# Performance work log

Hardware: AMD Instinct MI355X
Metric: run time of the kernel (lower is better)

The kernel has to match this reference:

```python
import jax, jax.numpy as jnp
import numpy as np
from jax import lax

SCALES = (1, 4, 16, 64)
EPS = 1e-5
B, S, D, H, R, FF = 4, 1024, 512, 8, 4, 2048
C = D // len(SCALES)  # channels per temporal scale


def _ln(x, g, b):
    mu = jnp.mean(x, -1, keepdims=True)
    var = jnp.mean(jnp.square(x - mu), -1, keepdims=True)
    return (x - mu) * lax.rsqrt(var + EPS) * g + b


def _interp_linear(y, L_out):
    # y: [B, C, L_in]; torch F.interpolate(mode='linear', align_corners=False)
    L_in = y.shape[-1]
    if L_in == L_out:
        return y
    pos = (jnp.arange(L_out, dtype=jnp.float32) + 0.5) * (L_in / L_out) - 0.5
    pos = jnp.clip(pos, 0.0, L_in - 1)
    lo = jnp.floor(pos).astype(jnp.int32)
    hi = jnp.minimum(lo + 1, L_in - 1)
    w = (pos - lo.astype(jnp.float32))
    return y[..., lo] * (1.0 - w) + y[..., hi] * w


def _conv1d(x, w, b, stride):
    # x: [B, Cin, L], w: [Cout, Cin, K]
    y = lax.conv_general_dilated(x, w, window_strides=(stride,), padding='VALID',
                                 dimension_numbers=('NCH', 'OIH', 'NCH'))
    return y + b[None, :, None]


def setup_inputs() -> dict:
    key = jax.random.key(0)
    ks = jax.random.split(key, 40)
    n = lambda k, shp, s=0.02: jax.random.normal(k, shp, jnp.float32) * s
    inp = {}
    inp['x'] = jax.random.normal(ks[0], (B, S, D), jnp.float32)
    inp['resource_mask'] = jax.random.randint(ks[1], (B, S), 0, R, jnp.int32)
    inp['attention_mask'] = jnp.ones((B, S), jnp.int32)
    inp['wq'] = n(ks[2], (D, D)); inp['bq'] = jnp.zeros((D,), jnp.float32)
    inp['wk'] = n(ks[3], (D, D)); inp['bk'] = jnp.zeros((D,), jnp.float32)
    inp['wv'] = n(ks[4], (D, D)); inp['bv'] = jnp.zeros((D,), jnp.float32)
    inp['wo'] = n(ks[5], (D, D)); inp['bo'] = jnp.zeros((D,), jnp.float32)
    inp['rbias'] = jax.random.normal(ks[6], (H, R, R), jnp.float32)
    for i, sc in enumerate(SCALES):
        inp[f'cw{i}'] = n(ks[7 + i], (C, D, sc))
        inp[f'cb{i}'] = jnp.zeros((C,), jnp.float32)
    inp['fw'] = n(ks[12], (D, D)); inp['fb'] = jnp.zeros((D,), jnp.float32)
    inp['ltg'] = jnp.ones((D,), jnp.float32); inp['ltb'] = jnp.zeros((D,), jnp.float32)
    inp['n1g'] = jnp.ones((D,), jnp.float32); inp['n1b'] = jnp.zeros((D,), jnp.float32)
    inp['n2g'] = jnp.ones((D,), jnp.float32); inp['n2b'] = jnp.zeros((D,), jnp.float32)
    inp['fw1'] = n(ks[13], (FF, D)); inp['fb1'] = jnp.zeros((FF,), jnp.float32)
    inp['fw2'] = n(ks[14], (D, FF)); inp['fb2'] = jnp.zeros((D,), jnp.float32)
    inp['n3g'] = jnp.ones((D,), jnp.float32); inp['n3b'] = jnp.zeros((D,), jnp.float32)
    return inp


def reference(x, resource_mask, attention_mask, wq, bq, wk, bk, wv, bv, wo, bo, rbias,
              cw0, cb0, cw1, cb1, cw2, cb2, cw3, cb3, fw, fb, ltg, ltb,
              n1g, n1b, n2g, n2b, fw1, fb1, fw2, fb2, n3g, n3b):
    b_, s_, d_ = x.shape
    dk = d_ // H
    # --- ResourceAwareAttention (dropout = identity in eval) ---
    q = (x @ wq.T + bq).reshape(b_, s_, H, dk).transpose(0, 2, 1, 3)
    k = (x @ wk.T + bk).reshape(b_, s_, H, dk).transpose(0, 2, 1, 3)
    v = (x @ wv.T + bv).reshape(b_, s_, H, dk).transpose(0, 2, 1, 3)
    scores = jnp.einsum('bhid,bhjd->bhij', q, k) / jnp.sqrt(jnp.float32(dk))
    # vectorized resource-bias gather: bias[b,h,i,j] = rbias[h, rm[b,i], rm[b,j]]
    idx_h = jnp.arange(H)[None, :, None, None]
    idx_i = resource_mask[:, None, :, None]
    idx_j = resource_mask[:, None, None, :]
    scores = scores + rbias[idx_h, idx_i, idx_j]
    scores = jnp.where(attention_mask[:, None, None, :] == 0, -1e9, scores)
    attn = jax.nn.softmax(scores, axis=-1)
    o = jnp.einsum('bhij,bhjd->bhid', attn, v).transpose(0, 2, 1, 3).reshape(b_, s_, d_)
    attn_out = o @ wo.T + bo
    x = _ln(x + attn_out, n1g, n1b)
    # --- MultiScaleTemporalEncoder ---
    xc = x.transpose(0, 2, 1)  # [B, D, S]
    convs = ((cw0, cb0), (cw1, cb1), (cw2, cb2), (cw3, cb3))
    outs = []
    for sc, (w, bb) in zip(SCALES, convs):
        y = _conv1d(xc, w, bb, sc)  # [B, C, S/sc]
        outs.append(_interp_linear(y, s_))
    ms = jnp.concatenate(outs, axis=1).transpose(0, 2, 1)  # [B, S, D]
    fused = ms @ fw.T + fb
    temporal = _ln(x + fused, ltg, ltb)
    x = _ln(x + temporal, n2g, n2b)
    # --- FFN ---
    ff = jax.nn.relu(x @ fw1.T + fb1) @ fw2.T + fb2
    return _ln(x + ff, n3g, n3b)
```

## Files before the change

### kernel.cpp

```cpp
#include <hip/hip_runtime.h>
#include <math.h>

constexpr int B_ = 4, S_ = 1024, D_ = 512, H_ = 8, FF_ = 2048;
constexpr int DK_ = 64;
constexpr int C_ = 128;
constexpr int QKVLD = 1536;

typedef __bf16 bf16x8 __attribute__((ext_vector_type(8)));
typedef __bf16 bf16x4 __attribute__((ext_vector_type(4)));
typedef short short4v __attribute__((ext_vector_type(4)));
typedef float floatx4 __attribute__((ext_vector_type(4)));

__device__ __forceinline__ void g2l16(const __bf16* g, __bf16* l) {
  __builtin_amdgcn_global_load_lds(
      (__attribute__((address_space(1))) void*)(unsigned long long)g,
      (__attribute__((address_space(3))) void*)(unsigned int)(unsigned long long)l,
      16, 0, 0);
}

__device__ __forceinline__ int xcd_swz(int lin, int nwg) {
  return (lin & 7) * (nwg >> 3) + (lin >> 3);
}

template <bool OUTBF16, bool RELU, bool WRITEVT>
__global__ __launch_bounds__(256, 2) void mgemm(
    const __bf16* __restrict__ A, const __bf16* __restrict__ W,
    const float* __restrict__ bias, void* __restrict__ Yv,
    int M, int N, int K, int ldY, __bf16* __restrict__ VT) {
  __shared__ __bf16 As[2][128 * 64];
  __shared__ __bf16 Bs[2][128 * 64];
  const int tid = threadIdx.x;
  const int wave = tid >> 6, lane = tid & 63;
  const int nwg = gridDim.x * gridDim.y;
  const int lin = blockIdx.y * gridDim.x + blockIdx.x;
  const int swz = xcd_swz(lin, nwg);
  const int bm = (swz / gridDim.x) * 128, bn = (swz % gridDim.x) * 128;

  const int rsub = lane >> 3;
  const int gch = ((lane & 7) ^ rsub) * 8;
  const __bf16* gA = A + (size_t)(bm + wave * 32 + rsub) * K + gch;
  const __bf16* gB = W + (size_t)(bn + wave * 32 + rsub) * K + gch;

  const int mrow = lane & 15, g4 = lane >> 4;
  const int rsw = mrow & 7;
  const int wm = (wave & 1) * 64, wn = (wave >> 1) * 64;

  floatx4 acc[4][4];
#pragma unroll
  for (int mi = 0; mi < 4; mi++)
#pragma unroll
    for (int ni = 0; ni < 4; ni++) acc[mi][ni] = (floatx4){0.f, 0.f, 0.f, 0.f};

  const int nk = K >> 6;
  auto stage = [&](int buf, int kt) {
    const __bf16* ga = gA + (size_t)kt * 64;
    const __bf16* gb = gB + (size_t)kt * 64;
    __bf16* la = &As[buf][wave * 32 * 64];
    __bf16* lb = &Bs[buf][wave * 32 * 64];
#pragma unroll
    for (int i = 0; i < 4; i++) {
      g2l16(ga + (size_t)(i * 8) * K, la + i * 8 * 64);
      g2l16(gb + (size_t)(i * 8) * K, lb + i * 8 * 64);
    }
  };

  stage(0, 0);
  int cur = 0;
  for (int kk = 0; kk < nk; kk++) {
    __syncthreads();
    if (kk + 1 < nk) stage(cur ^ 1, kk + 1);
    const __bf16* Ab = As[cur];
    const __bf16* Bb = Bs[cur];
#pragma unroll
    for (int c = 0; c < 2; c++) {
      const int pc = (((c * 4 + g4) ^ rsw)) * 8;
      bf16x8 af[4], bfr[4];
#pragma unroll
      for (int mi = 0; mi < 4; mi++)
        af[mi] = *(const bf16x8*)(Ab + (wm + mi * 16 + mrow) * 64 + pc);
#pragma unroll
      for (int ni = 0; ni < 4; ni++)
        bfr[ni] = *(const bf16x8*)(Bb + (wn + ni * 16 + mrow) * 64 + pc);
#pragma unroll
      for (int mi = 0; mi < 4; mi++)
#pragma unroll
        for (int ni = 0; ni < 4; ni++)
          acc[mi][ni] = __builtin_amdgcn_mfma_f32_16x16x32_bf16(af[mi], bfr[ni], acc[mi][ni], 0, 0, 0);
    }
    cur ^= 1;
  }

  const int cc = lane & 15;
  const int r0 = (lane >> 4) * 4;
  float bv[4];
#pragma unroll
  for (int ni = 0; ni < 4; ni++) bv[ni] = bias[bn + wn + ni * 16 + cc];
#pragma unroll
  for (int mi = 0; mi < 4; mi++) {
#pragma unroll
    for (int ni = 0; ni < 4; ni++) {
      const int col = bn + wn + ni * 16 + cc;
      if (WRITEVT && col >= 1024) {
        const int h = (col - 1024) >> 6, d = (col - 1024) & 63;
        const int rowb = bm + wm + mi * 16 + r0;
        const int b = rowb >> 10, s = rowb & 1023;
        union { __bf16 hh[4]; unsigned long long u; } w;
#pragma unroll
        for (int i = 0; i < 4; i++) w.hh[i] = (__bf16)(acc[mi][ni][i] + bv[ni]);
        *(unsigned long long*)(VT + (size_t)(b * 8 + h) * 65536 + (size_t)d * 1024 + s) = w.u;
      } else {
#pragma unroll
        for (int i = 0; i < 4; i++) {
          float v = acc[mi][ni][i] + bv[ni];
          if (RELU) v = fmaxf(v, 0.f);
          const size_t row = bm + wm + mi * 16 + r0 + i;
          if (OUTBF16)
            ((__bf16*)Yv)[row * ldY + col] = (__bf16)v;
          else
            ((float*)Yv)[row * ldY + col] = v;
        }
      }
    }
  }
}

__global__ __launch_bounds__(256, 4) void mgemm64s(
    const __bf16* __restrict__ A, const __bf16* __restrict__ W,
    float* __restrict__ Y0, float* __restrict__ Y1,
    int Kstride, int Khalf) {
  __shared__ __bf16 As[2][64 * 64];
  __shared__ __bf16 Bs[2][64 * 64];
  const int tid = threadIdx.x;
  const int wave = tid >> 6, lane = tid & 63;
  const int nwg = gridDim.x * gridDim.y;
  const int lin = blockIdx.y * gridDim.x + blockIdx.x;
  const int swz = xcd_swz(lin, nwg);
  const int bn = (swz & 7) * 64;
  const int rest = swz >> 3;
  const int ks = rest & 1;
  const int bm = (rest >> 1) * 64;
  const int k0 = ks * Khalf;
  float* __restrict__ Y = ks ? Y1 : Y0;

  const int rsub = lane >> 3;
  const int gch = ((lane & 7) ^ rsub) * 8;
  const __bf16* gA = A + (size_t)(bm + wave * 16 + rsub) * Kstride + k0 + gch;
  const __bf16* gB = W + (size_t)(bn + wave * 16 + rsub) * Kstride + k0 + gch;

  const int mrow = lane & 15, g4 = lane >> 4;
  const int rsw = mrow & 7;
  const int wm = (wave & 1) * 32, wn = (wave >> 1) * 32;

  floatx4 acc[2][2];
#pragma unroll
  for (int mi = 0; mi < 2; mi++)
#pragma unroll
    for (int ni = 0; ni < 2; ni++) acc[mi][ni] = (floatx4){0.f, 0.f, 0.f, 0.f};

  const int nk = Khalf >> 6;
  auto stage = [&](int buf, int kt) {
    const __bf16* ga = gA + (size_t)kt * 64;
    const __bf16* gb = gB + (size_t)kt * 64;
    __bf16* la = &As[buf][wave * 16 * 64];
    __bf16* lb = &Bs[buf][wave * 16 * 64];
#pragma unroll
    for (int i = 0; i < 2; i++) {
      g2l16(ga + (size_t)(i * 8) * Kstride, la + i * 8 * 64);
      g2l16(gb + (size_t)(i * 8) * Kstride, lb + i * 8 * 64);
    }
  };

  stage(0, 0);
  int cur = 0;
  for (int kk = 0; kk < nk; kk++) {
    __syncthreads();
    if (kk + 1 < nk) stage(cur ^ 1, kk + 1);
    const __bf16* Ab = As[cur];
    const __bf16* Bb = Bs[cur];
#pragma unroll
    for (int c = 0; c < 2; c++) {
      const int pc = (((c * 4 + g4) ^ rsw)) * 8;
      bf16x8 af[2], bfr[2];
#pragma unroll
      for (int mi = 0; mi < 2; mi++)
        af[mi] = *(const bf16x8*)(Ab + (wm + mi * 16 + mrow) * 64 + pc);
#pragma unroll
      for (int ni = 0; ni < 2; ni++)
        bfr[ni] = *(const bf16x8*)(Bb + (wn + ni * 16 + mrow) * 64 + pc);
#pragma unroll
      for (int mi = 0; mi < 2; mi++)
#pragma unroll
        for (int ni = 0; ni < 2; ni++)
          acc[mi][ni] = __builtin_amdgcn_mfma_f32_16x16x32_bf16(af[mi], bfr[ni], acc[mi][ni], 0, 0, 0);
    }
    cur ^= 1;
  }

  const int cc = lane & 15;
  const int r0 = (lane >> 4) * 4;
#pragma unroll
  for (int mi = 0; mi < 2; mi++) {
#pragma unroll
    for (int ni = 0; ni < 2; ni++) {
      const int col = bn + wn + ni * 16 + cc;
#pragma unroll
      for (int i = 0; i < 4; i++) {
        const size_t row = bm + wm + mi * 16 + r0 + i;
        Y[row * 512 + col] = acc[mi][ni][i];
      }
    }
  }
}

__global__ __launch_bounds__(256, 2) void cgemm3(
    const __bf16* __restrict__ A, const __bf16* __restrict__ w4,
    const __bf16* __restrict__ w16, const __bf16* __restrict__ w64,
    const __bf16* __restrict__ w1, const float* __restrict__ cb0,
    float* __restrict__ y1, float* __restrict__ y2, float* __restrict__ y3,
    __bf16* __restrict__ msb) {
  int id = xcd_swz(blockIdx.x, 448);
  const __bf16* W;
  float* yseg = nullptr;
  int K, bm, k0, nk;
  bool direct = false;
  if (id < 128) {
    W = w4; yseg = y1; K = 2048; bm = (id & 15) * 64; k0 = (id >> 4) * 256; nk = 4;
  } else if (id < 256) {
    id -= 128;
    W = w16; yseg = y2; K = 8192; bm = (id & 3) * 64; k0 = (id >> 2) * 256; nk = 4;
  } else if (id < 384) {
    id -= 256;
    W = w64; yseg = y3; K = 32768; bm = 0; k0 = id * 256; nk = 4;
  } else {
    id -= 384;
    W = w1; K = 512; bm = id * 64; k0 = 0; nk = 8; direct = true;
  }

  __shared__ __bf16 As[2][64 * 64];
  __shared__ __bf16 Bs[2][128 * 64];
  const int tid = threadIdx.x;
  const int wave = tid >> 6, lane = tid & 63;

  const int rsub = lane >> 3;
  const int gch = ((lane & 7) ^ rsub) * 8;
  const __bf16* gA = A + (size_t)(bm + wave * 16 + rsub) * K + k0 + gch;
  const __bf16* gB = W + (size_t)(wave * 32 + rsub) * K + k0 + gch;

  const int mrow = lane & 15, g4 = lane >> 4;
  const int rsw = mrow & 7;

  floatx4 acc[8];
#pragma unroll
  for (int nj = 0; nj < 8; nj++) acc[nj] = (floatx4){0.f, 0.f, 0.f, 0.f};

  auto stage = [&](int buf, int kt) {
    const size_t ko = (size_t)kt * 64;
#pragma unroll
    for (int i = 0; i < 2; i++)
      g2l16(gA + ko + (size_t)(i * 8) * K, &As[buf][(wave * 16 + i * 8) * 64]);
#pragma unroll
    for (int i = 0; i < 4; i++)
      g2l16(gB + ko + (size_t)(i * 8) * K, &Bs[buf][(wave * 32 + i * 8) * 64]);
  };

  stage(0, 0);
  int cur = 0;
  for (int kk = 0; kk < nk; kk++) {
    __syncthreads();
    if (kk + 1 < nk) stage(cur ^ 1, kk + 1);
    const __bf16* Ab = As[cur];
    const __bf16* Bb = Bs[cur];
#pragma unroll
    for (int c = 0; c < 2; c++) {
      const int pc = (((c * 4 + g4) ^ rsw)) * 8;
      bf16x8 af = *(const bf16x8*)(Ab + (wave * 16 + mrow) * 64 + pc);
#pragma unroll
      for (int nj = 0; nj < 8; nj++) {
        bf16x8 bfv = *(const bf16x8*)(Bb + (nj * 16 + mrow) * 64 + pc);
        acc[nj] = __builtin_amdgcn_mfma_f32_16x16x32_bf16(af, bfv, acc[nj], 0, 0, 0);
      }
    }
    cur ^= 1;
  }

  const int cc = lane & 15;
  const int r0 = (lane >> 4) * 4;
  if (direct) {
#pragma unroll
    for (int nj = 0; nj < 8; nj++) {
      const float bb = cb0[nj * 16 + cc];
#pragma unroll
      for (int i = 0; i < 4; i++)
        msb[(size_t)(bm + wave * 16 + r0 + i) * 512 + nj * 16 + cc] =
            (__bf16)(acc[nj][i] + bb);
    }
  } else {
#pragma unroll
    for (int nj = 0; nj < 8; nj++)
#pragma unroll
      for (int i = 0; i < 4; i++)
        atomicAdd(&yseg[(size_t)(bm + wave * 16 + r0 + i) * 128 + nj * 16 + cc],
                  acc[nj][i]);
  }
}

__global__ __launch_bounds__(256) void prep(
    const float* __restrict__ cw1, const float* __restrict__ cw2,
    const float* __restrict__ cw3, __bf16* __restrict__ wt4,
    __bf16* __restrict__ wt16, __bf16* __restrict__ wt64,
    const float* __restrict__ s0, const float* __restrict__ s1,
    const float* __restrict__ s2, const float* __restrict__ s3,
    const float* __restrict__ s4, const float* __restrict__ s5,
    const float* __restrict__ s6, const float* __restrict__ s7,
    const float* __restrict__ s8,
    __bf16* __restrict__ d0, __bf16* __restrict__ d1, __bf16* __restrict__ d2,
    __bf16* __restrict__ d3, __bf16* __restrict__ d4, __bf16* __restrict__ d5,
    __bf16* __restrict__ d6, __bf16* __restrict__ d7, __bf16* __restrict__ d8,
    const float* __restrict__ bq, const float* __restrict__ bk,
    const float* __restrict__ bv, float* __restrict__ bqkv,
    const float* __restrict__ cb1, const float* __restrict__ cb2,
    const float* __restrict__ cb3, float* __restrict__ yall) {
  __shared__ float Ts[4608];
  const int tid = threadIdx.x;
  if (blockIdx.x < 1408) {
    int id = blockIdx.x;
    const float* cw;
    __bf16* wt;
    int lg, c, d0i, TD, L;
    if (id < 128) {
      cw = cw1; wt = wt4; lg = 2; c = id; d0i = 0; TD = 512; L = 2048;
    } else if (id < 384) {
      id -= 128;
      cw = cw2; wt = wt16; lg = 4; c = id >> 1; d0i = (id & 1) * 256; TD = 256; L = 4096;
    } else {
      id -= 384;
      cw = cw3; wt = wt64; lg = 6; c = id >> 3; d0i = (id & 7) * 64; TD = 64; L = 4096;
    }
    const int sc = 1 << lg;
    const int KD = 512 << lg;
    const float* src = cw + (size_t)c * KD + (size_t)d0i * sc;

    for (int f = tid * 4; f < L; f += 1024) {
      const float4 v = *(const float4*)(src + f);
      const float vv[4] = {v.x, v.y, v.z, v.w};
#pragma unroll
      for (int j = 0; j < 4; j++) {
        const int idx = f + j;
        const int dl = idx >> lg, k = idx & (sc - 1);
        Ts[dl * (sc + 1) + k] = vv[j];
      }
    }
    __syncthreads();

    for (int w = tid * 8; w < L; w += 2048) {
      const int kpos = w / TD;
      const int dl0 = w - kpos * TD;
      union { __bf16 hh[8]; bf16x8 v; } u;
#pragma unroll
      for (int j = 0; j < 8; j++)
        u.hh[j] = (__bf16)Ts[(dl0 + j) * (sc + 1) + kpos];
      *(bf16x8*)(wt + (size_t)c * KD + kpos * 512 + d0i + dl0) = u.v;
    }
    return;
  }

  const int qd = (blockIdx.x - 1408) * 256 + tid;
  if (qd < 384) {
    const int i = qd * 4;
    const float* s;
    int off;
    if (i < 512) { s = bq; off = 0; }
    else if (i < 1024) { s = bk; off = 512; }
    else { s = bv; off = 1024; }
    *(float4*)(bqkv + i) = *(const float4*)(s + i - off);
  }
  if (qd < 172032) {
    float bb;
    if (qd < 131072) bb = cb1[qd & 127];
    else if (qd < 163840) bb = cb2[qd & 127];
    else bb = cb3[qd & 127];
    yall[qd] = bb;
  }
  if (qd >= 1392640) return;
  const float* src;
  __bf16* dst;
  int base;
  if (qd < 524288) { src = s0; dst = d0; base = 0; }
  else if (qd < 589824) { src = s1; dst = d1; base = 524288; }
  else if (qd < 655360) { src = s2; dst = d2; base = 589824; }
  else if (qd < 720896) { src = s3; dst = d3; base = 655360; }
  else if (qd < 786432) { src = s4; dst = d4; base = 720896; }
  else if (qd < 851968) { src = s5; dst = d5; base = 786432; }
  else if (qd < 868352) { src = s6; dst = d6; base = 851968; }
  else if (qd < 1130496) { src = s7; dst = d7; base = 868352; }
  else { src = s8; dst = d8; base = 1130496; }
  const int local = qd - base;
  float4 v = *(const float4*)(src + (size_t)local * 4);
  union { __bf16 h[4]; unsigned long long u; } t;
  t.h[0] = (__bf16)v.x; t.h[1] = (__bf16)v.y;
  t.h[2] = (__bf16)v.z; t.h[3] = (__bf16)v.w;
  *(unsigned long long*)(dst + (size_t)local * 4) = t.u;
}

__global__ __launch_bounds__(256) void fattn(
    const __bf16* __restrict__ QKV, const __bf16* __restrict__ VT,
    const float* __restrict__ rbias, const int* __restrict__ rm,
    const int* __restrict__ amask, __bf16* __restrict__ O) {
  __shared__ __bf16 Ks[2][64 * 64];
  __shared__ __bf16 Vs[2][64 * 64];
  __shared__ float T[4 * 1032];

  const int tid = threadIdx.x, wave = tid >> 6, lane = tid & 63;
  const int nwg = gridDim.x * gridDim.y;
  const int lin = blockIdx.y * gridDim.x + blockIdx.x;
  const int swz = xcd_swz(lin, nwg);
  const int qb = swz % gridDim.x;
  const int bh = swz / gridDim.x;
  const int b = bh >> 3, h = bh & 7;
  const int q0 = qb * 64;
  const int cc = lane & 15, quad = lane >> 4;

  for (int j = tid; j < 1024; j += 256) {
    const int rv = rm[b * S_ + j];
    const float mk = amask[b * S_ + j] ? 1.f : 0.f;
#pragma unroll
    for (int ri = 0; ri < 4; ri++)
      T[ri * 1032 + j] = __expf(rbias[h * 16 + ri * 4 + rv]) * mk;
  }

  const int qrow = q0 + wave * 16;
  const int rmi = rm[b * S_ + qrow + cc];
  const float* Trow = T + rmi * 1032;

  const __bf16* Qr = QKV + (size_t)(b * S_ + qrow + cc) * QKVLD + h * 64;
  const bf16x8 qb0 = *(const bf16x8*)(Qr + quad * 8);
  const bf16x8 qb1 = *(const bf16x8*)(Qr + 32 + quad * 8);

  floatx4 of[4];
#pragma unroll
  for (int dc = 0; dc < 4; dc++) of[dc] = (floatx4){0.f, 0.f, 0.f, 0.f};
  float mold = -1e30f, l = 0.f;

  const int rsub = lane >> 3;
  const int sgch = ((lane & 7) ^ rsub) * 8;
  const __bf16* Kg = QKV + (size_t)(b * S_ + wave * 16 + rsub) * QKVLD + 512 + h * 64 + sgch;
  const __bf16* Vg = VT + (size_t)bh * 65536 + (size_t)(wave * 16 + rsub) * 1024 + sgch;

  auto stage = [&](int buf, int jt) {
    const int j0 = jt * 64;
#pragma unroll
    for (int i = 0; i < 2; i++) {
      g2l16(Kg + (size_t)(j0 + i * 8) * QKVLD, &Ks[buf][(wave * 16 + i * 8) * 64]);
      g2l16(Vg + j0 + (size_t)(i * 8) * 1024, &Vs[buf][(wave * 16 + i * 8) * 64]);
    }
  };

  stage(0, 0);
  int cur = 0;
  const int rk = cc & 7;

  for (int jt = 0; jt < 16; jt++) {
    const int j0 = jt * 64;
    __syncthreads();
    if (jt + 1 < 16) stage(cur ^ 1, jt + 1);
    const __bf16* Kb = Ks[cur];
    const __bf16* Vb = Vs[cur];

    floatx4 st[4];
    __builtin_amdgcn_s_setprio(1);
#pragma unroll
    for (int js = 0; js < 4; js++) {
      const bf16x8 ka0 = *(const bf16x8*)(Kb + (js * 16 + cc) * 64 + ((quad ^ rk) * 8));
      const bf16x8 ka1 = *(const bf16x8*)(Kb + (js * 16 + cc) * 64 + (((quad + 4) ^ rk) * 8));
      floatx4 s = (floatx4){0.f, 0.f, 0.f, 0.f};
      s = __builtin_amdgcn_mfma_f32_16x16x32_bf16(ka0, qb0, s, 0, 0, 0);
      s = __builtin_amdgcn_mfma_f32_16x16x32_bf16(ka1, qb1, s, 0, 0, 0);
      st[js] = s;
    }
    __builtin_amdgcn_s_setprio(0);

    float mxr = st[0][0];
#pragma unroll
    for (int js = 0; js < 4; js++)
#pragma unroll
      for (int i = 0; i < 4; i++) mxr = fmaxf(mxr, st[js][i]);
    mxr = fmaxf(mxr, __shfl_xor(mxr, 16));
    mxr = fmaxf(mxr, __shfl_xor(mxr, 32));
    const float mnew = fmaxf(mold, mxr * 0.125f);
    const float alpha = __expf(mold - mnew);
    mold = mnew;

    float rsum = 0.f;
    short4v pk[4];
#pragma unroll
    for (int js = 0; js < 4; js++) {
      const floatx4 Tv = *(const floatx4*)(Trow + j0 + js * 16 + quad * 4);
      union { __bf16 hh[4]; short4v s4; } u;
#pragma unroll
      for (int i = 0; i < 4; i++) {
        const float p = __expf(fmaf(st[js][i], 0.125f, -mnew)) * Tv[i];
        rsum += p;
        u.hh[i] = (__bf16)p;
      }
      pk[js] = u.s4;
    }
    rsum += __shfl_xor(rsum, 16);
    rsum += __shfl_xor(rsum, 32);
    l = l * alpha + rsum;

#pragma unroll
    for (int dc = 0; dc < 4; dc++)
#pragma unroll
      for (int i = 0; i < 4; i++) of[dc][i] *= alpha;

    __builtin_amdgcn_s_setprio(1);
#pragma unroll
    for (int dc = 0; dc < 4; dc++) {
#pragma unroll
      for (int js = 0; js < 4; js++) {
        union { bf16x4 v; short4v s4; } va;
        va.v = *(const bf16x4*)(Vb + (dc * 16 + cc) * 64 +
                                (((js * 2 + (quad >> 1)) ^ rk) * 8) + (quad & 1) * 4);
        of[dc] = __builtin_amdgcn_mfma_f32_16x16x16bf16_1k(va.s4, pk[js], of[dc], 0, 0, 0);
      }
    }
    __builtin_amdgcn_s_setprio(0);
    cur ^= 1;
  }

  const float invl = 1.f / l;
  __bf16* po = O + (size_t)(b * S_ + qrow + cc) * D_ + h * 64;
#pragma unroll
  for (int dc = 0; dc < 4; dc++) {
    union { __bf16 hh[4]; unsigned long long u; } w;
#pragma unroll
    for (int i = 0; i < 4; i++) w.hh[i] = (__bf16)(of[dc][i] * invl);
    *(unsigned long long*)(po + dc * 16 + quad * 4) = w.u;
  }
}

__global__ __launch_bounds__(256) void add_ln_kernel(
    const float* __restrict__ xa, const float* __restrict__ h0,
    const float* __restrict__ h1, const float* __restrict__ bias,
    const float* __restrict__ g, const float* __restrict__ be,
    float* __restrict__ out, __bf16* __restrict__ outb) {
  const int row = (blockIdx.x * 256 + threadIdx.x) >> 6;
  const int lane = threadIdx.x & 63;
  const floatx4* pa = (const floatx4*)(xa + (size_t)row * D_);
  const floatx4* p0 = (const floatx4*)(h0 + (size_t)row * D_);
  const floatx4* p1 = (const floatx4*)(h1 + (size_t)row * D_);
  floatx4 v[2];
  float sum = 0.f;
#pragma unroll
  for (int i = 0; i < 2; i++) {
    const int dd = lane + 64 * i;
    v[i] = pa[dd] + p0[dd] + p1[dd] + ((const floatx4*)bias)[dd];
    sum += v[i][0] + v[i][1] + v[i][2] + v[i][3];
  }
#pragma unroll
  for (int off = 32; off; off >>= 1) sum += __shfl_xor(sum, off);
  const float mu = sum * (1.f / D_);
  float vs = 0.f;
#pragma unroll
  for (int i = 0; i < 2; i++)
#pragma unroll
    for (int j = 0; j < 4; j++) { float t = v[i][j] - mu; vs += t * t; }
#pragma unroll
  for (int off = 32; off; off >>= 1) vs += __shfl_xor(vs, off);
  const float inv = rsqrtf(vs * (1.f / D_) + 1e-5f);
  floatx4* po = (floatx4*)(out + (size_t)row * D_);
#pragma unroll
  for (int i = 0; i < 2; i++) {
    const int dd = lane + 64 * i;
    const floatx4 g4 = ((const floatx4*)g)[dd];
    const floatx4 b4 = ((const floatx4*)be)[dd];
    const floatx4 o = (v[i] - mu) * inv * g4 + b4;
    po[dd] = o;
    if (outb) {
      union { __bf16 hh[4]; unsigned long long u; } w;
#pragma unroll
      for (int j = 0; j < 4; j++) w.hh[j] = (__bf16)o[j];
      *(unsigned long long*)(outb + (size_t)row * D_ + dd * 4) = w.u;
    }
  }
}

__global__ __launch_bounds__(256) void ln_chain_kernel(
    const float* __restrict__ x1, const float* __restrict__ h0,
    const float* __restrict__ h1, const float* __restrict__ bias,
    const float* __restrict__ ltg, const float* __restrict__ ltb,
    const float* __restrict__ n2g, const float* __restrict__ n2b,
    float* __restrict__ out, __bf16* __restrict__ outb) {
  const int row = (blockIdx.x * 256 + threadIdx.x) >> 6;
  const int lane = threadIdx.x & 63;
  const floatx4* p1 = (const floatx4*)(x1 + (size_t)row * D_);
  const floatx4* pf0 = (const floatx4*)(h0 + (size_t)row * D_);
  const floatx4* pf1 = (const floatx4*)(h1 + (size_t)row * D_);
  floatx4 xv[2], u[2];
  float sum = 0.f;
#pragma unroll
  for (int i = 0; i < 2; i++) {
    const int dd = lane + 64 * i;
    xv[i] = p1[dd];
    u[i] = xv[i] + pf0[dd] + pf1[dd] + ((const floatx4*)bias)[dd];
    sum += u[i][0] + u[i][1] + u[i][2] + u[i][3];
  }
#pragma unroll
  for (int off = 32; off; off >>= 1) sum += __shfl_xor(sum, off);
  float mu = sum * (1.f / D_);
  float vs = 0.f;
#pragma unroll
  for (int i = 0; i < 2; i++)
#pragma unroll
    for (int j = 0; j < 4; j++) { float t = u[i][j] - mu; vs += t * t; }
#pragma unroll
  for (int off = 32; off; off >>= 1) vs += __shfl_xor(vs, off);
  float inv = rsqrtf(vs * (1.f / D_) + 1e-5f);
  float sum2 = 0.f;
#pragma unroll
  for (int i = 0; i < 2; i++) {
    const int dd = lane + 64 * i;
    const floatx4 g4 = ((const floatx4*)ltg)[dd];
    const floatx4 b4 = ((const floatx4*)ltb)[dd];
    u[i] = xv[i] + ((u[i] - mu) * inv * g4 + b4);
    sum2 += u[i][0] + u[i][1] + u[i][2] + u[i][3];
  }
#pragma unroll
  for (int off = 32; off; off >>= 1) sum2 += __shfl_xor(sum2, off);
  float mu2 = sum2 * (1.f / D_);
  float vs2 = 0.f;
#pragma unroll
  for (int i = 0; i < 2; i++)
#pragma unroll
    for (int j = 0; j < 4; j++) { float t = u[i][j] - mu2; vs2 += t * t; }
#pragma unroll
  for (int off = 32; off; off >>= 1) vs2 += __shfl_xor(vs2, off);
  float inv2 = rsqrtf(vs2 * (1.f / D_) + 1e-5f);
  floatx4* po = (floatx4*)(out + (size_t)row * D_);
#pragma unroll
  for (int i = 0; i < 2; i++) {
    const int dd = lane + 64 * i;
    const floatx4 g4 = ((const floatx4*)n2g)[dd];
    const floatx4 b4 = ((const floatx4*)n2b)[dd];
    const floatx4 o = (u[i] - mu2) * inv2 * g4 + b4;
    po[dd] = o;
    union { __bf16 hh[4]; unsigned long long u8; } w;
#pragma unroll
    for (int j = 0; j < 4; j++) w.hh[j] = (__bf16)o[j];
    *(unsigned long long*)(outb + (size_t)row * D_ + dd * 4) = w.u8;
  }
}

__global__ void interp_kernel(const float* __restrict__ y1, const float* __restrict__ y2,
                              const float* __restrict__ y3, __bf16* __restrict__ ms) {
  int idx = blockIdx.x * 256 + threadIdx.x;
  if (idx >= B_ * S_ * 3 * C_ / 4) return;
  const int c3_4 = idx % 96;
  const int rest = idx / 96;
  const int s = rest & 1023, b = rest >> 10;
  const int i = c3_4 >> 5;
  const int c = (c3_4 & 31) * 4;
  const int Lin = (i == 0) ? 256 : (i == 1) ? 64 : 16;
  const float* y = (i == 0) ? y1 : (i == 1) ? y2 : y3;
  float pos = (s + 0.5f) * ((float)Lin / S_) - 0.5f;
  pos = fminf(fmaxf(pos, 0.f), (float)(Lin - 1));
  const int lo = (int)floorf(pos);
  const int hi = min(lo + 1, Lin - 1);
  const float w = pos - (float)lo;
  const float* ybase = y + ((size_t)(b * Lin + lo)) * 128 + c;
  const floatx4 vlo = *(const floatx4*)ybase;
  const floatx4 vhi = *(const floatx4*)(ybase + (size_t)(hi - lo) * 128);
  const floatx4 o = vlo * (1.f - w) + vhi * w;
  union { __bf16 hh[4]; unsigned long long u; } t;
#pragma unroll
  for (int j = 0; j < 4; j++) t.hh[j] = (__bf16)o[j];
  *(unsigned long long*)(ms + ((size_t)b * S_ + s) * D_ + C_ + i * 128 + c) = t.u;
}

extern "C" void kernel_launch(void* const* d_in, const int* in_sizes, int n_in,
                              void* d_out, int out_size, void* d_ws, size_t ws_size,
                              hipStream_t stream) {
  const float* x   = (const float*)d_in[0];
  const int* rm    = (const int*)d_in[1];
  const int* am    = (const int*)d_in[2];
  const float* wq  = (const float*)d_in[3];
  const float* bq  = (const float*)d_in[4];
  const float* wk  = (const float*)d_in[5];
  const float* bk  = (const float*)d_in[6];
  const float* wv  = (const float*)d_in[7];
  const float* bv  = (const float*)d_in[8];
  const float* wo  = (const float*)d_in[9];
  const float* bo  = (const float*)d_in[10];
  const float* rbias = (const float*)d_in[11];
  const float* cw0 = (const float*)d_in[12];
  const float* cb0 = (const float*)d_in[13];
  const float* cw1 = (const float*)d_in[14];
  const float* cb1 = (const float*)d_in[15];
  const float* cw2 = (const float*)d_in[16];
  const float* cb2 = (const float*)d_in[17];
  const float* cw3 = (const float*)d_in[18];
  const float* cb3 = (const float*)d_in[19];
  const float* fw  = (const float*)d_in[20];
  const float* fb  = (const float*)d_in[21];
  const float* ltg = (const float*)d_in[22];
  const float* ltb = (const float*)d_in[23];
  const float* n1g = (const float*)d_in[24];
  const float* n1b = (const float*)d_in[25];
  const float* n2g = (const float*)d_in[26];
  const float* n2b = (const float*)d_in[27];
  const float* fw1 = (const float*)d_in[28];
  const float* fb1 = (const float*)d_in[29];
  const float* fw2 = (const float*)d_in[30];
  const float* fb2 = (const float*)d_in[31];
  const float* n3g = (const float*)d_in[32];
  const float* n3b = (const float*)d_in[33];

  float* ws = (float*)d_ws;
  __bf16* wqkvb = (__bf16*)(ws + 0);
  __bf16* wob   = (__bf16*)(ws + 393216);
  __bf16* fwb   = (__bf16*)(ws + 524288);
  __bf16* cw0b  = (__bf16*)(ws + 655360);
  __bf16* fw1b  = (__bf16*)(ws + 688128);
  __bf16* fw2b  = (__bf16*)(ws + 1212416);
  __bf16* xb    = (__bf16*)(ws + 1835008);
  __bf16* qkv   = (__bf16*)(ws + 2883584);
  __bf16* attnb = (__bf16*)(ws + 6029312);
  float*  x1    = ws + 7077888;
  __bf16* x1b   = (__bf16*)(ws + 9175040);
  float*  scr   = ws + 10223616;
  float*  x2    = ws + 12320768;
  __bf16* x2b   = (__bf16*)(ws + 14417920);
  __bf16* msb   = (__bf16*)(ws + 15466496);
  float*  y1    = ws + 16515072;
  float*  y2    = ws + 16646144;
  float*  y3    = ws + 16678912;
  float*  bqkv  = ws + 16687104;
  __bf16* wt4b  = (__bf16*)(ws + 16689152);
  __bf16* wt16b = (__bf16*)(ws + 16820224);
  __bf16* wt64b = (__bf16*)(ws + 17344512);
  __bf16* VT    = (__bf16*)(ws + 10223616);
  __bf16* ffh   = (__bf16*)(ws + 2883584);
  float*  h1a   = ws + 2883584;

  dim3 blk(256);

  prep<<<6848, blk, 0, stream>>>(
      cw1, cw2, cw3, wt4b, wt16b, wt64b,
      x, wq, wk, wv, wo, fw, cw0, fw1, fw2,
      xb, wqkvb, wqkvb + 262144, wqkvb + 524288, wob, fwb, cw0b, fw1b, fw2b,
      bq, bk, bv, bqkv, cb1, cb2, cb3, y1);

  mgemm<true, false, true><<<dim3(12, 32), blk, 0, stream>>>(
      xb, wqkvb, bqkv, qkv, 4096, 1536, 512, QKVLD, VT);

  fattn<<<dim3(16, 32), blk, 0, stream>>>(qkv, VT, rbias, rm, am, attnb);

  mgemm64s<<<dim3(8, 128), blk, 0, stream>>>(attnb, wob, scr, h1a, 512, 256);
  add_ln_kernel<<<1024, blk, 0, stream>>>(x, scr, h1a, bo, n1g, n1b, x1, x1b);

  cgemm3<<<448, blk, 0, stream>>>(x1b, wt4b, wt16b, wt64b, cw0b, cb0, y1, y2, y3, msb);
  interp_kernel<<<1536, blk, 0, stream>>>(y1, y2, y3, msb);

  mgemm64s<<<dim3(8, 128), blk, 0, stream>>>(msb, fwb, scr, h1a, 512, 256);
  ln_chain_kernel<<<1024, blk, 0, stream>>>(x1, scr, h1a, fb, ltg, ltb, n2g, n2b, x2, x2b);

  mgemm<true, true, false><<<dim3(16, 32), blk, 0, stream>>>(
      x2b, fw1b, fb1, ffh, 4096, 2048, 512, 2048, nullptr);
  mgemm64s<<<dim3(8, 128), blk, 0, stream>>>(ffh, fw2b, scr, x1, 2048, 1024);
  add_ln_kernel<<<1024, blk, 0, stream>>>(x2, scr, x1, fb2, n3g, n3b, (float*)d_out, nullptr);
}
```

Before: 268.9 us.

## Split prep kernel and co-schedule weight conversion with flash attention

The monolithic prep kernel is split in two. A small prepA converts only x and the QKV weights and biases needed by the first GEMM. The remaining weight conversions (conv weight transposes, wo/fw/fw1/fw2 casts, bias init) are appended as extra blocks to the attention kernel, so they can fill idle CUs alongside attention work instead of sitting on the critical path before it. Separately, cgemm3's split-K for the scale-16 and scale-64 convolutions is made coarser (fewer blocks, longer K per block), which reduces atomic adds at the cost of less parallelism.

```diff
diff --git a/kernel.cpp b/kernel.cpp
--- a/kernel.cpp
+++ b/kernel.cpp
@@ -218,21 +218,21 @@
     const __bf16* __restrict__ w1, const float* __restrict__ cb0,
     float* __restrict__ y1, float* __restrict__ y2, float* __restrict__ y3,
     __bf16* __restrict__ msb) {
-  int id = xcd_swz(blockIdx.x, 448);
+  int id = xcd_swz(blockIdx.x, 288);
   const __bf16* W;
   float* yseg = nullptr;
   int K, bm, k0, nk;
   bool direct = false;
   if (id < 128) {
     W = w4; yseg = y1; K = 2048; bm = (id & 15) * 64; k0 = (id >> 4) * 256; nk = 4;
-  } else if (id < 256) {
+  } else if (id < 192) {
     id -= 128;
-    W = w16; yseg = y2; K = 8192; bm = (id & 3) * 64; k0 = (id >> 2) * 256; nk = 4;
-  } else if (id < 384) {
-    id -= 256;
-    W = w64; yseg = y3; K = 32768; bm = 0; k0 = id * 256; nk = 4;
+    W = w16; yseg = y2; K = 8192; bm = (id & 3) * 64; k0 = (id >> 2) * 512; nk = 8;
+  } else if (id < 224) {
+    id -= 192;
+    W = w64; yseg = y3; K = 32768; bm = 0; k0 = id * 1024; nk = 16;
   } else {
-    id -= 384;
+    id -= 224;
     W = w1; K = 512; bm = id * 64; k0 = 0; nk = 8; direct = true;
   }
 
@@ -304,26 +304,192 @@
   }
 }
 
-__global__ __launch_bounds__(256) void prep(
+__global__ void prepA(
+    const float* __restrict__ x, const float* __restrict__ wq,
+    const float* __restrict__ wk, const float* __restrict__ wv,
+    __bf16* __restrict__ xb, __bf16* __restrict__ wqb,
+    __bf16* __restrict__ wkb, __bf16* __restrict__ wvb,
+    const float* __restrict__ bq, const float* __restrict__ bk,
+    const float* __restrict__ bv, float* __restrict__ bqkv) {
+  const int qd = blockIdx.x * 256 + threadIdx.x;
+  if (qd < 384) {
+    const int i = qd * 4;
+    const float* s;
+    int off;
+    if (i < 512) { s = bq; off = 0; }
+    else if (i < 1024) { s = bk; off = 512; }
+    else { s = bv; off = 1024; }
+    *(float4*)(bqkv + i) = *(const float4*)(s + i - off);
+  }
+  const float* src;
+  __bf16* dst;
+  int base;
+  if (qd < 524288) { src = x; dst = xb; base = 0; }
+  else if (qd < 589824) { src = wq; dst = wqb; base = 524288; }
+  else if (qd < 655360) { src = wk; dst = wkb; base = 589824; }
+  else { src = wv; dst = wvb; base = 655360; }
+  const int local = qd - base;
+  float4 v = *(const float4*)(src + (size_t)local * 4);
+  union { __bf16 h[4]; unsigned long long u; } t;
+  t.h[0] = (__bf16)v.x; t.h[1] = (__bf16)v.y;
+  t.h[2] = (__bf16)v.z; t.h[3] = (__bf16)v.w;
+  *(unsigned long long*)(dst + (size_t)local * 4) = t.u;
+}
+
+__global__ __launch_bounds__(256) void fattnP(
+    const __bf16* __restrict__ QKV, const __bf16* __restrict__ VT,
+    const float* __restrict__ rbias, const int* __restrict__ rm,
+    const int* __restrict__ amask, __bf16* __restrict__ O,
     const float* __restrict__ cw1, const float* __restrict__ cw2,
     const float* __restrict__ cw3, __bf16* __restrict__ wt4,
     __bf16* __restrict__ wt16, __bf16* __restrict__ wt64,
-    const float* __restrict__ s0, const float* __restrict__ s1,
-    const float* __restrict__ s2, const float* __restrict__ s3,
     const float* __restrict__ s4, const float* __restrict__ s5,
     const float* __restrict__ s6, const float* __restrict__ s7,
     const float* __restrict__ s8,
-    __bf16* __restrict__ d0, __bf16* __restrict__ d1, __bf16* __restrict__ d2,
-    __bf16* __restrict__ d3, __bf16* __restrict__ d4, __bf16* __restrict__ d5,
-    __bf16* __restrict__ d6, __bf16* __restrict__ d7, __bf16* __restrict__ d8,
-    const float* __restrict__ bq, const float* __restrict__ bk,
-    const float* __restrict__ bv, float* __restrict__ bqkv,
+    __bf16* __restrict__ d4, __bf16* __restrict__ d5, __bf16* __restrict__ d6,
+    __bf16* __restrict__ d7, __bf16* __restrict__ d8,
     const float* __restrict__ cb1, const float* __restrict__ cb2,
     const float* __restrict__ cb3, float* __restrict__ yall) {
-  __shared__ float Ts[4608];
+  __shared__ __align__(16) char smraw[49280];
   const int tid = threadIdx.x;
-  if (blockIdx.x < 1408) {
-    int id = blockIdx.x;
+
+  if (blockIdx.x < 512) {
+    __bf16* KsB = (__bf16*)smraw;
+    __bf16* VsB = KsB + 8192;
+    float* T = (float*)(smraw + 32768);
+
+    const int wave = tid >> 6, lane = tid & 63;
+    const int swz = xcd_swz((int)blockIdx.x, 512);
+    const int qb = swz % 16;
+    const int bh = swz / 16;
+    const int b = bh >> 3, h = bh & 7;
+    const int q0 = qb * 64;
+    const int cc = lane & 15, quad = lane >> 4;
+
+    for (int j = tid; j < 1024; j += 256) {
+      const int rv = rm[b * S_ + j];
+      const float mk = amask[b * S_ + j] ? 1.f : 0.f;
+#pragma unroll
+      for (int ri = 0; ri < 4; ri++)
+        T[ri * 1032 + j] = __expf(rbias[h * 16 + ri * 4 + rv]) * mk;
+    }
+
+    const int qrow = q0 + wave * 16;
+    const int rmi = rm[b * S_ + qrow + cc];
+    const float* Trow = T + rmi * 1032;
+
+    const __bf16* Qr = QKV + (size_t)(b * S_ + qrow + cc) * QKVLD + h * 64;
+    const bf16x8 qb0 = *(const bf16x8*)(Qr + quad * 8);
+    const bf16x8 qb1 = *(const bf16x8*)(Qr + 32 + quad * 8);
+
+    floatx4 of[4];
+#pragma unroll
+    for (int dc = 0; dc < 4; dc++) of[dc] = (floatx4){0.f, 0.f, 0.f, 0.f};
+    float mold = -1e30f, l = 0.f;
+
+    const int rsub = lane >> 3;
+    const int sgch = ((lane & 7) ^ rsub) * 8;
+    const __bf16* Kg = QKV + (size_t)(b * S_ + wave * 16 + rsub) * QKVLD + 512 + h * 64 + sgch;
+    const __bf16* Vg = VT + (size_t)bh * 65536 + (size_t)(wave * 16 + rsub) * 1024 + sgch;
+
+    auto stage = [&](int buf, int jt) {
+      const int j0 = jt * 64;
+#pragma unroll
+      for (int i = 0; i < 2; i++) {
+        g2l16(Kg + (size_t)(j0 + i * 8) * QKVLD, KsB + buf * 4096 + (wave * 16 + i * 8) * 64);
+        g2l16(Vg + j0 + (size_t)(i * 8) * 1024, VsB + buf * 4096 + (wave * 16 + i * 8) * 64);
+      }
+    };
+
+    stage(0, 0);
+    int cur = 0;
+    const int rk = cc & 7;
+
+    for (int jt = 0; jt < 16; jt++) {
+      const int j0 = jt * 64;
+      __syncthreads();
+      if (jt + 1 < 16) stage(cur ^ 1, jt + 1);
+      const __bf16* Kb = KsB + cur * 4096;
+      const __bf16* Vb = VsB + cur * 4096;
+
+      floatx4 st[4];
+      __builtin_amdgcn_s_setprio(1);
+#pragma unroll
+      for (int js = 0; js < 4; js++) {
+        const bf16x8 ka0 = *(const bf16x8*)(Kb + (js * 16 + cc) * 64 + ((quad ^ rk) * 8));
+        const bf16x8 ka1 = *(const bf16x8*)(Kb + (js * 16 + cc) * 64 + (((quad + 4) ^ rk) * 8));
+        floatx4 s = (floatx4){0.f, 0.f, 0.f, 0.f};
+        s = __builtin_amdgcn_mfma_f32_16x16x32_bf16(ka0, qb0, s, 0, 0, 0);
+        s = __builtin_amdgcn_mfma_f32_16x16x32_bf16(ka1, qb1, s, 0, 0, 0);
+        st[js] = s;
+      }
+      __builtin_amdgcn_s_setprio(0);
+
+      float mxr = st[0][0];
+#pragma unroll
+      for (int js = 0; js < 4; js++)
+#pragma unroll
+        for (int i = 0; i < 4; i++) mxr = fmaxf(mxr, st[js][i]);
+      mxr = fmaxf(mxr, __shfl_xor(mxr, 16));
+      mxr = fmaxf(mxr, __shfl_xor(mxr, 32));
+      const float mnew = fmaxf(mold, mxr * 0.125f);
+      const float alpha = __expf(mold - mnew);
+      mold = mnew;
+
+      float rsum = 0.f;
+      short4v pk[4];
+#pragma unroll
+      for (int js = 0; js < 4; js++) {
+        const floatx4 Tv = *(const floatx4*)(Trow + j0 + js * 16 + quad * 4);
+        union { __bf16 hh[4]; short4v s4v; } u;
+#pragma unroll
+        for (int i = 0; i < 4; i++) {
+          const float p = __expf(fmaf(st[js][i], 0.125f, -mnew)) * Tv[i];
+          rsum += p;
+          u.hh[i] = (__bf16)p;
+        }
+        pk[js] = u.s4v;
+      }
+      rsum += __shfl_xor(rsum, 16);
+      rsum += __shfl_xor(rsum, 32);
+      l = l * alpha + rsum;
+
+#pragma unroll
+      for (int dc = 0; dc < 4; dc++)
+#pragma unroll
+        for (int i = 0; i < 4; i++) of[dc][i] *= alpha;
+
+      __builtin_amdgcn_s_setprio(1);
+#pragma unroll
+      for (int dc = 0; dc < 4; dc++) {
+#pragma unroll
+        for (int js = 0; js < 4; js++) {
+          union { bf16x4 v; short4v s4v; } va;
+          va.v = *(const bf16x4*)(Vb + (dc * 16 + cc) * 64 +
+                                  (((js * 2 + (quad >> 1)) ^ rk) * 8) + (quad & 1) * 4);
+          of[dc] = __builtin_amdgcn_mfma_f32_16x16x16bf16_1k(va.s4v, pk[js], of[dc], 0, 0, 0);
+        }
+      }
+      __builtin_amdgcn_s_setprio(0);
+      cur ^= 1;
+    }
+
+    const float invl = 1.f / l;
+    __bf16* po = O + (size_t)(b * S_ + qrow + cc) * D_ + h * 64;
+#pragma unroll
+    for (int dc = 0; dc < 4; dc++) {
+      union { __bf16 hh[4]; unsigned long long u; } w;
+#pragma unroll
+      for (int i = 0; i < 4; i++) w.hh[i] = (__bf16)(of[dc][i] * invl);
+      *(unsigned long long*)(po + dc * 16 + quad * 4) = w.u;
+    }
+    return;
+  }
+
+  int pb = blockIdx.x - 512;
+  if (pb < 1408) {
+    float* Ts = (float*)smraw;
+    int id = pb;
     const float* cw;
     __bf16* wt;
     int lg, c, d0i, TD, L;
@@ -364,16 +530,7 @@
     return;
   }
 
-  const int qd = (blockIdx.x - 1408) * 256 + tid;
-  if (qd < 384) {
-    const int i = qd * 4;
-    const float* s;
-    int off;
-    if (i < 512) { s = bq; off = 0; }
-    else if (i < 1024) { s = bk; off = 512; }
-    else { s = bv; off = 1024; }
-    *(float4*)(bqkv + i) = *(const float4*)(s + i - off);
-  }
+  const int qd = (pb - 1408) * 256 + tid;
   if (qd < 172032) {
     float bb;
     if (qd < 131072) bb = cb1[qd & 127];
@@ -381,162 +538,20 @@
     else bb = cb3[qd & 127];
     yall[qd] = bb;
   }
-  if (qd >= 1392640) return;
   const float* src;
   __bf16* dst;
   int base;
-  if (qd < 524288) { src = s0; dst = d0; base = 0; }
-  else if (qd < 589824) { src = s1; dst = d1; base = 524288; }
-  else if (qd < 655360) { src = s2; dst = d2; base = 589824; }
-  else if (qd < 720896) { src = s3; dst = d3; base = 655360; }
-  else if (qd < 786432) { src = s4; dst = d4; base = 720896; }
-  else if (qd < 851968) { src = s5; dst = d5; base = 786432; }
-  else if (qd < 868352) { src = s6; dst = d6; base = 851968; }
-  else if (qd < 1130496) { src = s7; dst = d7; base = 868352; }
-  else { src = s8; dst = d8; base = 1130496; }
+  if (qd < 65536) { src = s4; dst = d4; base = 0; }
+  else if (qd < 131072) { src = s5; dst = d5; base = 65536; }
+  else if (qd < 147456) { src = s6; dst = d6; base = 131072; }
+  else if (qd < 409600) { src = s7; dst = d7; base = 147456; }
+  else { src = s8; dst = d8; base = 409600; }
   const int local = qd - base;
   float4 v = *(const float4*)(src + (size_t)local * 4);
   union { __bf16 h[4]; unsigned long long u; } t;
   t.h[0] = (__bf16)v.x; t.h[1] = (__bf16)v.y;
   t.h[2] = (__bf16)v.z; t.h[3] = (__bf16)v.w;
   *(unsigned long long*)(dst + (size_t)local * 4) = t.u;
-}
-
-__global__ __launch_bounds__(256) void fattn(
-    const __bf16* __restrict__ QKV, const __bf16* __restrict__ VT,
-    const float* __restrict__ rbias, const int* __restrict__ rm,
-    const int* __restrict__ amask, __bf16* __restrict__ O) {
-  __shared__ __bf16 Ks[2][64 * 64];
-  __shared__ __bf16 Vs[2][64 * 64];
-  __shared__ float T[4 * 1032];
-
-  const int tid = threadIdx.x, wave = tid >> 6, lane = tid & 63;
-  const int nwg = gridDim.x * gridDim.y;
-  const int lin = blockIdx.y * gridDim.x + blockIdx.x;
-  const int swz = xcd_swz(lin, nwg);
-  const int qb = swz % gridDim.x;
-  const int bh = swz / gridDim.x;
-  const int b = bh >> 3, h = bh & 7;
-  const int q0 = qb * 64;
-  const int cc = lane & 15, quad = lane >> 4;
-
-  for (int j = tid; j < 1024; j += 256) {
-    const int rv = rm[b * S_ + j];
-    const float mk = amask[b * S_ + j] ? 1.f : 0.f;
-#pragma unroll
-    for (int ri = 0; ri < 4; ri++)
-      T[ri * 1032 + j] = __expf(rbias[h * 16 + ri * 4 + rv]) * mk;
-  }
-
-  const int qrow = q0 + wave * 16;
-  const int rmi = rm[b * S_ + qrow + cc];
-  const float* Trow = T + rmi * 1032;
-
-  const __bf16* Qr = QKV + (size_t)(b * S_ + qrow + cc) * QKVLD + h * 64;
-  const bf16x8 qb0 = *(const bf16x8*)(Qr + quad * 8);
-  const bf16x8 qb1 = *(const bf16x8*)(Qr + 32 + quad * 8);
-
-  floatx4 of[4];
-#pragma unroll
-  for (int dc = 0; dc < 4; dc++) of[dc] = (floatx4){0.f, 0.f, 0.f, 0.f};
-  float mold = -1e30f, l = 0.f;
-
-  const int rsub = lane >> 3;
-  const int sgch = ((lane & 7) ^ rsub) * 8;
-  const __bf16* Kg = QKV + (size_t)(b * S_ + wave * 16 + rsub) * QKVLD + 512 + h * 64 + sgch;
-  const __bf16* Vg = VT + (size_t)bh * 65536 + (size_t)(wave * 16 + rsub) * 1024 + sgch;
-
-  auto stage = [&](int buf, int jt) {
-    const int j0 = jt * 64;
-#pragma unroll
-    for (int i = 0; i < 2; i++) {
-      g2l16(Kg + (size_t)(j0 + i * 8) * QKVLD, &Ks[buf][(wave * 16 + i * 8) * 64]);
-      g2l16(Vg + j0 + (size_t)(i * 8) * 1024, &Vs[buf][(wave * 16 + i * 8) * 64]);
-    }
-  };
-
-  stage(0, 0);
-  int cur = 0;
-  const int rk = cc & 7;
-
-  for (int jt = 0; jt < 16; jt++) {
-    const int j0 = jt * 64;
-    __syncthreads();
-    if (jt + 1 < 16) stage(cur ^ 1, jt + 1);
-    const __bf16* Kb = Ks[cur];
-    const __bf16* Vb = Vs[cur];
-
-    floatx4 st[4];
-    __builtin_amdgcn_s_setprio(1);
-#pragma unroll
-    for (int js = 0; js < 4; js++) {
-      const bf16x8 ka0 = *(const bf16x8*)(Kb + (js * 16 + cc) * 64 + ((quad ^ rk) * 8));
-      const bf16x8 ka1 = *(const bf16x8*)(Kb + (js * 16 + cc) * 64 + (((quad + 4) ^ rk) * 8));
-      floatx4 s = (floatx4){0.f, 0.f, 0.f, 0.f};
-      s = __builtin_amdgcn_mfma_f32_16x16x32_bf16(ka0, qb0, s, 0, 0, 0);
-      s = __builtin_amdgcn_mfma_f32_16x16x32_bf16(ka1, qb1, s, 0, 0, 0);
-      st[js] = s;
-    }
-    __builtin_amdgcn_s_setprio(0);
-
-    float mxr = st[0][0];
-#pragma unroll
-    for (int js = 0; js < 4; js++)
-#pragma unroll
-      for (int i = 0; i < 4; i++) mxr = fmaxf(mxr, st[js][i]);
-    mxr = fmaxf(mxr, __shfl_xor(mxr, 16));
-    mxr = fmaxf(mxr, __shfl_xor(mxr, 32));
-    const float mnew = fmaxf(mold, mxr * 0.125f);
-    const float alpha = __expf(mold - mnew);
-    mold = mnew;
-
-    float rsum = 0.f;
-    short4v pk[4];
-#pragma unroll
-    for (int js = 0; js < 4; js++) {
-      const floatx4 Tv = *(const floatx4*)(Trow + j0 + js * 16 + quad * 4);
-      union { __bf16 hh[4]; short4v s4; } u;
-#pragma unroll
-      for (int i = 0; i < 4; i++) {
-        const float p = __expf(fmaf(st[js][i], 0.125f, -mnew)) * Tv[i];
-        rsum += p;
-        u.hh[i] = (__bf16)p;
-      }
-      pk[js] = u.s4;
-    }
-    rsum += __shfl_xor(rsum, 16);
-    rsum += __shfl_xor(rsum, 32);
-    l = l * alpha + rsum;
-
-#pragma unroll
-    for (int dc = 0; dc < 4; dc++)
-#pragma unroll
-      for (int i = 0; i < 4; i++) of[dc][i] *= alpha;
-
-    __builtin_amdgcn_s_setprio(1);
-#pragma unroll
-    for (int dc = 0; dc < 4; dc++) {
-#pragma unroll
-      for (int js = 0; js < 4; js++) {
-        union { bf16x4 v; short4v s4; } va;
-        va.v = *(const bf16x4*)(Vb + (dc * 16 + cc) * 64 +
-                                (((js * 2 + (quad >> 1)) ^ rk) * 8) + (quad & 1) * 4);
-        of[dc] = __builtin_amdgcn_mfma_f32_16x16x16bf16_1k(va.s4, pk[js], of[dc], 0, 0, 0);
-      }
-    }
-    __builtin_amdgcn_s_setprio(0);
-    cur ^= 1;
-  }
-
-  const float invl = 1.f / l;
-  __bf16* po = O + (size_t)(b * S_ + qrow + cc) * D_ + h * 64;
-#pragma unroll
-  for (int dc = 0; dc < 4; dc++) {
-    union { __bf16 hh[4]; unsigned long long u; } w;
-#pragma unroll
-    for (int i = 0; i < 4; i++) w.hh[i] = (__bf16)(of[dc][i] * invl);
-    *(unsigned long long*)(po + dc * 16 + quad * 4) = w.u;
-  }
 }
 
 __global__ __launch_bounds__(256) void add_ln_kernel(
@@ -744,21 +759,25 @@
 
   dim3 blk(256);
 
-  prep<<<6848, blk, 0, stream>>>(
-      cw1, cw2, cw3, wt4b, wt16b, wt64b,
-      x, wq, wk, wv, wo, fw, cw0, fw1, fw2,
-      xb, wqkvb, wqkvb + 262144, wqkvb + 524288, wob, fwb, cw0b, fw1b, fw2b,
-      bq, bk, bv, bqkv, cb1, cb2, cb3, y1);
+  prepA<<<2816, blk, 0, stream>>>(
+      x, wq, wk, wv,
+      xb, wqkvb, wqkvb + 262144, wqkvb + 524288,
+      bq, bk, bv, bqkv);
 
   mgemm<true, false, true><<<dim3(12, 32), blk, 0, stream>>>(
       xb, wqkvb, bqkv, qkv, 4096, 1536, 512, QKVLD, VT);
 
-  fattn<<<dim3(16, 32), blk, 0, stream>>>(qkv, VT, rbias, rm, am, attnb);
+  fattnP<<<4544, blk, 0, stream>>>(
+      qkv, VT, rbias, rm, am, attnb,
+      cw1, cw2, cw3, wt4b, wt16b, wt64b,
+      wo, fw, cw0, fw1, fw2,
+      wob, fwb, cw0b, fw1b, fw2b,
+      cb1, cb2, cb3, y1);
 
   mgemm64s<<<dim3(8, 128), blk, 0, stream>>>(attnb, wob, scr, h1a, 512, 256);
   add_ln_kernel<<<1024, blk, 0, stream>>>(x, scr, h1a, bo, n1g, n1b, x1, x1b);
 
-  cgemm3<<<448, blk, 0, stream>>>(x1b, wt4b, wt16b, wt64b, cw0b, cb0, y1, y2, y3, msb);
+  cgemm3<<<288, blk, 0, stream>>>(x1b, wt4b, wt16b, wt64b, cw0b, cb0, y1, y2, y3, msb);
   interp_kernel<<<1536, blk, 0, stream>>>(y1, y2, y3, msb);
 
   mgemm64s<<<dim3(8, 128), blk, 0, stream>>>(msb, fwb, scr, h1a, 512, 256);
```

Result: faster. 262.6 us (-2.4%).
